# Kernel optimization log

Measured on AMD Instinct MI355X. Metric: run time of the kernel, lower is better.

Reference implementation:

```python
import jax, jax.numpy as jnp
import numpy as np

B, T, D = 8, 2048, 1024
EPS = 1e-5

def _layernorm(x, g, b):
    mu = jnp.mean(x, axis=-1, keepdims=True)
    var = jnp.mean(jnp.square(x - mu), axis=-1, keepdims=True)
    return (x - mu) * jax.lax.rsqrt(var + EPS) * g + b

def setup_inputs() -> dict:
    key = jax.random.key(0)
    ks = jax.random.split(key, 8)
    scale = 1.0 / np.sqrt(D)
    text_inputs = jax.random.normal(ks[0], (B, T, D), dtype=jnp.float32)
    sit_mask = jax.random.randint(ks[1], (B, T), 0, 2).astype(jnp.float32)
    Wq = jax.random.normal(ks[2], (D, D), dtype=jnp.float32) * scale
    Wk = jax.random.normal(ks[3], (D, D), dtype=jnp.float32) * scale
    Wv = jax.random.normal(ks[4], (D, D), dtype=jnp.float32) * scale
    Wf1 = jax.random.normal(ks[5], (D, D), dtype=jnp.float32) * scale
    bf1 = jnp.zeros((D,), dtype=jnp.float32)
    Wf2 = jax.random.normal(ks[6], (D, D), dtype=jnp.float32) * scale
    bf2 = jnp.zeros((D,), dtype=jnp.float32)
    ln1_g = jnp.ones((D,), dtype=jnp.float32)
    ln1_b = jnp.zeros((D,), dtype=jnp.float32)
    ln2_g = jnp.ones((D,), dtype=jnp.float32)
    ln2_b = jnp.zeros((D,), dtype=jnp.float32)
    return dict(text_inputs=text_inputs, sit_mask=sit_mask, Wq=Wq, Wk=Wk, Wv=Wv,
                ln1_g=ln1_g, ln1_b=ln1_b, Wf1=Wf1, bf1=bf1, Wf2=Wf2, bf2=bf2,
                ln2_g=ln2_g, ln2_b=ln2_b)

def reference(text_inputs, sit_mask, Wq, Wk, Wv, ln1_g, ln1_b, Wf1, bf1, Wf2, bf2, ln2_g, ln2_b):
    x = text_inputs  # [B,T,D]
    d = x.shape[-1]
    # torch Linear: y = x @ W.T
    q = jnp.einsum('btd,ed->bte', x, Wq)
    k = jnp.einsum('btd,ed->bte', x, Wk)
    v = jnp.einsum('btd,ed->bte', x, Wv)
    # scaled scores with causal (strictly-upper = -inf) mask
    scores = jnp.einsum('btd,bsd->bts', q, k) / jnp.sqrt(jnp.asarray(d, x.dtype))
    causal = jnp.tril(jnp.ones((x.shape[1], x.shape[1]), dtype=bool))  # keep diag + past
    scores = jnp.where(causal[None], scores, -jnp.inf)
    attn = jax.nn.softmax(scores, axis=-1)
    # per-batch SIT padding mask applied AFTER softmax (rows may not sum to 1)
    pad_keep = (sit_mask[:, :, None] * sit_mask[:, None, :]) != 0  # [B,T,T]
    attn = jnp.where(pad_keep, attn, 0.0)
    att_out = jnp.einsum('bts,bsd->btd', attn, v)
    # residual + LN, FFN (Linear-ReLU-Linear), residual + LN
    h = _layernorm(att_out + x, ln1_g, ln1_b)
    ff = jnp.einsum('btd,ed->bte', jax.nn.relu(jnp.einsum('btd,ed->bte', h, Wf1) + bf1), Wf2) + bf2
    out = _layernorm(ff + h, ln2_g, ln2_b)
    return out
```

## Files before the change

### kernel.cpp

```cpp
#include <hip/hip_runtime.h>

typedef unsigned short ushort_t;
typedef __attribute__((ext_vector_type(8))) __bf16 bf16x8;
typedef __attribute__((ext_vector_type(4))) float f32x4;
typedef __attribute__((ext_vector_type(4))) int i32x4;
typedef __attribute__((ext_vector_type(4))) unsigned short u16x4;

__device__ __forceinline__ float bf2f(ushort_t u) {
  union { unsigned u32; float f; } c; c.u32 = ((unsigned)u) << 16; return c.f;
}
__device__ __forceinline__ ushort_t f2bf(float f) {
  union { float f; unsigned u32; } c; c.f = f;
  unsigned u = c.u32;
  u += 0x7fffu + ((u >> 16) & 1u);
  return (ushort_t)(u >> 16);
}

__device__ __forceinline__ void gload_lds16(const void* g, void* l) {
  __builtin_amdgcn_global_load_lds(
      (const __attribute__((address_space(1))) void*)g,
      (__attribute__((address_space(3))) void*)l,
      16, 0, 0);
}

__device__ __forceinline__ void stage_half(const char* gbase, long row0, int ldbytes,
                                           int kbyte, char* lds_half, int tid)
{
  const int rl = tid >> 3;
  const int cs = ((tid & 7) ^ (rl & 7)) << 4;
  const char* g0 = gbase + (row0 + rl) * (long)ldbytes + kbyte + cs;
  char* l0 = lds_half + ((tid >> 6) << 10);
  gload_lds16(g0, l0);
  gload_lds16(g0 + (long)ldbytes * 64, l0 + 8192);
}

#define FENCE() asm volatile("" ::: "memory")
#define BARX() do { FENCE(); __builtin_amdgcn_sched_barrier(0); \
  __builtin_amdgcn_s_barrier(); __builtin_amdgcn_sched_barrier(0); FENCE(); } while (0)
#define VMW4() do { FENCE(); asm volatile("s_waitcnt vmcnt(4)" ::: "memory"); FENCE(); } while (0)
#define PR1() __builtin_amdgcn_s_setprio(1)
#define PR0() __builtin_amdgcn_s_setprio(0)

#define READ_A(dst, Abase, mb) \
  _Pragma("unroll") for (int m_ = 0; m_ < 4; ++m_) { \
    const char* p_ = (Abase) + ((wr << 7) + (mb) + m_ * 16 + fr) * 128; \
    dst[m_][0] = *(const bf16x8*)(p_ + ch0); \
    dst[m_][1] = *(const bf16x8*)(p_ + ch1); }

#define READ_B(dst, Bbase, jb) \
  _Pragma("unroll") for (int n_ = 0; n_ < 2; ++n_) { \
    const char* p_ = (Bbase) + ((wc << 6) + (jb) + n_ * 16 + fr) * 128; \
    dst[n_][0] = *(const bf16x8*)(p_ + ch0); \
    dst[n_][1] = *(const bf16x8*)(p_ + ch1); }

#define MFMA_Q(ib, jb, aarr, barr) \
  _Pragma("unroll") for (int m_ = 0; m_ < 4; ++m_) \
  _Pragma("unroll") for (int n_ = 0; n_ < 2; ++n_) \
  _Pragma("unroll") for (int s_ = 0; s_ < 2; ++s_) \
    acc[(ib) + m_][(jb) + n_] = __builtin_amdgcn_mfma_f32_16x16x32_bf16( \
        aarr[m_][s_], barr[n_][s_], acc[(ib) + m_][(jb) + n_], 0, 0, 0);

#define STAGE_A(t, h, db) stage_half(gA, m0 + (h) * 128, ldab, (t) << 7, \
    (char*)lds + (db) * 32768 + (h) * 16384, tid)
#define STAGE_B(t, h, db) stage_half(gB, n0 + (h) * 128, ldbb, (t) << 7, \
    (char*)lds + 65536 + (db) * 32768 + (h) * 16384, tid)

template<int EPI, bool TRI, bool CKLIM>
__global__ __launch_bounds__(512, 2) void gemm256(
    const ushort_t* __restrict__ A, int lda, long bsA,
    const ushort_t* __restrict__ B, int ldb, long bsB,
    ushort_t* __restrict__ C, int ldc, long bsC,
    const float* __restrict__ bias, float scale, int K)
{
  __shared__ __attribute__((aligned(16))) ushort_t lds[65536];

  int bx, by;
  if (TRI) {
    int bid = blockIdx.x; by = 0;
    while ((by + 1) * (by + 2) / 2 <= bid) ++by;
    bx = bid - by * (by + 1) / 2;
  } else { bx = blockIdx.x; by = blockIdx.y; }
  const int bz = blockIdx.z;
  const int NT = CKLIM ? ((by + 1) << 2) : (K >> 6);
  const int NIT = NT >> 1, NTm1 = NT - 1;

  const int tid = threadIdx.x;
  const int lane = tid & 63, fr = lane & 15, g = lane >> 4, lm = lane & 7;
  const int wv = tid >> 6, wr = wv >> 2, wc = wv & 3;
  const long m0 = (long)by << 8, n0 = (long)bx << 8;

  const char* gA = (const char*)(A + bz * bsA);
  const char* gB = (const char*)(B + bz * bsB);
  const int ldab = lda << 1, ldbb = ldb << 1;

  const int ch0 = (g ^ lm) << 4;
  const int ch1 = ((4 | g) ^ lm) << 4;

  const char* A0 = (const char*)lds;
  const char* A1 = (const char*)lds + 32768;
  const char* B0 = (const char*)lds + 65536;
  const char* B1 = (const char*)lds + 98304;

  f32x4 acc[8][4] = {};
  bf16x8 aF[4][2], aG[4][2], bX[2][2];

  STAGE_A(0, 0, 0); STAGE_A(0, 1, 0); STAGE_B(0, 0, 0); STAGE_B(0, 1, 0);
  STAGE_A(1, 0, 1); STAGE_A(1, 1, 1);
  VMW4(); BARX();

  for (int i = 0; i < NIT; ++i) {
    const int t1 = 2 * i + 1;
    const int t2 = (2 * i + 2 < NTm1) ? 2 * i + 2 : NTm1;
    const int t3 = (2 * i + 3 < NTm1) ? 2 * i + 3 : NTm1;

    READ_A(aF, A0, 0); READ_B(bX, B0, 0);
    STAGE_B(t1, 0, 1);
    BARX(); PR1(); MFMA_Q(0, 0, aF, bX); PR0(); BARX();
    READ_A(aG, A0, 64);
    STAGE_B(t1, 1, 1);
    BARX(); PR1(); MFMA_Q(4, 0, aG, bX); PR0(); BARX();
    READ_B(bX, B0, 32);
    STAGE_A(t2, 0, 0);
    BARX(); PR1(); MFMA_Q(4, 2, aG, bX); PR0(); BARX();
    STAGE_A(t2, 1, 0);
    BARX(); PR1(); MFMA_Q(0, 2, aF, bX); PR0(); VMW4(); BARX();
    READ_A(aF, A1, 0); READ_B(bX, B1, 0);
    STAGE_B(t2, 0, 0);
    BARX(); PR1(); MFMA_Q(0, 0, aF, bX); PR0(); BARX();
    READ_A(aG, A1, 64);
    STAGE_B(t2, 1, 0);
    BARX(); PR1(); MFMA_Q(4, 0, aG, bX); PR0(); BARX();
    READ_B(bX, B1, 32);
    STAGE_A(t3, 0, 1);
    BARX(); PR1(); MFMA_Q(4, 2, aG, bX); PR0(); BARX();
    STAGE_A(t3, 1, 1);
    BARX(); PR1(); MFMA_Q(0, 2, aF, bX); PR0(); VMW4(); BARX();
  }

  ushort_t* Cb = C + bz * bsC;
  const int cm = g << 2, cn = fr;
#pragma unroll
  for (int i2 = 0; i2 < 8; ++i2)
#pragma unroll
    for (int j2 = 0; j2 < 4; ++j2) {
      const long gm = m0 + (wr << 7) + i2 * 16 + cm;
      const long gn = n0 + (wc << 6) + j2 * 16 + cn;
      float bv = 0.f;
      if constexpr (EPI >= 1) bv = bias[gn];
#pragma unroll
      for (int r = 0; r < 4; ++r) {
        float v = acc[i2][j2][r] * scale + bv;
        if constexpr (EPI == 2) v = fmaxf(v, 0.f);
        Cb[(gm + r) * ldc + gn] = f2bf(v);
      }
    }
}

__global__ __launch_bounds__(256) void transpose_bf16(
    const ushort_t* __restrict__ V, int ldv, long bsV,
    ushort_t* __restrict__ Vt, int ldt, long bsT)
{
  __shared__ __attribute__((aligned(16))) ushort_t tile[64][72];
  const int bz = blockIdx.z;
  const ushort_t* Vb = V + bz * bsV;
  ushort_t* Tb = Vt + bz * bsT;
  const long s0 = (long)blockIdx.y << 6;
  const long d0 = (long)blockIdx.x << 6;
  const int tid = threadIdx.x;
  const int r = tid >> 3, c = tid & 7;
#pragma unroll
  for (int h = 0; h < 2; ++h) {
    const int rr = r + h * 32;
    i32x4 v = *(const i32x4*)(Vb + (s0 + rr) * ldv + d0 + c * 8);
    *(i32x4*)&tile[rr][c * 8] = v;
  }
  __syncthreads();
#pragma unroll
  for (int h = 0; h < 2; ++h) {
    const int dr = r + h * 32;
    union { ushort_t u[8]; i32x4 v; } t;
#pragma unroll
    for (int j = 0; j < 8; ++j) t.u[j] = tile[c * 8 + j][dr];
    *(i32x4*)(Tb + (d0 + dr) * ldt + s0 + c * 8) = t.v;
  }
}

__global__ __launch_bounds__(256) void softmax_sit(ushort_t* __restrict__ S,
                                                   const float* __restrict__ sit)
{
  __shared__ float buf[2048];
  __shared__ float red[4];
  const long row = blockIdx.x;
  const int b = (int)(row >> 11);
  const int t = (int)(row & 2047);
  ushort_t* Srow = S + (row << 11);
  const int tid = threadIdx.x;
  const int n = t + 1;

  float mloc = -3.0e38f;
  for (int i = tid; i < n; i += 256) {
    float v = bf2f(Srow[i]);
    buf[i] = v;
    mloc = fmaxf(mloc, v);
  }
#pragma unroll
  for (int o = 32; o > 0; o >>= 1) mloc = fmaxf(mloc, __shfl_down(mloc, o, 64));
  if ((tid & 63) == 0) red[tid >> 6] = mloc;
  __syncthreads();
  const float m = fmaxf(fmaxf(red[0], red[1]), fmaxf(red[2], red[3]));
  __syncthreads();

  float sloc = 0.f;
  for (int i = tid; i < n; i += 256) sloc += __expf(buf[i] - m);
#pragma unroll
  for (int o = 32; o > 0; o >>= 1) sloc += __shfl_down(sloc, o, 64);
  if ((tid & 63) == 0) red[tid >> 6] = sloc;
  __syncthreads();
  const float l = red[0] + red[1] + red[2] + red[3];

  float inv = 1.f / l;
  if (sit[row] == 0.f) inv = 0.f;
  const float* sitb = sit + ((long)b << 11);
  const int rup = ((t >> 8) + 1) << 8;
  for (int i = tid; i < rup; i += 256) {
    float p = 0.f;
    if (i < n && sitb[i] != 0.f) p = __expf(buf[i] - m) * inv;
    Srow[i] = f2bf(p);
  }
}

template<bool RES_F32, bool OUT_F32>
__global__ __launch_bounds__(256) void resid_ln(
    const ushort_t* __restrict__ xin, const void* __restrict__ resv,
    const float* __restrict__ g, const float* __restrict__ be, void* __restrict__ outv)
{
  __shared__ float red[4];
  const long base = (long)blockIdx.x << 10;
  const int tid = threadIdx.x;
  const int i0 = tid << 2;

  const u16x4 xa = *(const u16x4*)(xin + base + i0);
  float v[4];
  if constexpr (RES_F32) {
    const float4 rv = *(const float4*)((const float*)resv + base + i0);
    v[0] = bf2f(xa.x) + rv.x; v[1] = bf2f(xa.y) + rv.y;
    v[2] = bf2f(xa.z) + rv.z; v[3] = bf2f(xa.w) + rv.w;
  } else {
    const u16x4 rb = *(const u16x4*)((const ushort_t*)resv + base + i0);
    v[0] = bf2f(xa.x) + bf2f(rb.x); v[1] = bf2f(xa.y) + bf2f(rb.y);
    v[2] = bf2f(xa.z) + bf2f(rb.z); v[3] = bf2f(xa.w) + bf2f(rb.w);
  }
  float s = v[0] + v[1] + v[2] + v[3];
#pragma unroll
  for (int o = 32; o > 0; o >>= 1) s += __shfl_down(s, o, 64);
  if ((tid & 63) == 0) red[tid >> 6] = s;
  __syncthreads();
  const float mu = (red[0] + red[1] + red[2] + red[3]) * (1.f / 1024.f);
  __syncthreads();
  float s2 = 0.f;
#pragma unroll
  for (int j = 0; j < 4; ++j) { const float d = v[j] - mu; s2 += d * d; }
#pragma unroll
  for (int o = 32; o > 0; o >>= 1) s2 += __shfl_down(s2, o, 64);
  if ((tid & 63) == 0) red[tid >> 6] = s2;
  __syncthreads();
  const float rstd = rsqrtf((red[0] + red[1] + red[2] + red[3]) * (1.f / 1024.f) + 1e-5f);

  const float4 gv = *(const float4*)(g + i0);
  const float4 bv = *(const float4*)(be + i0);
  const float o0 = (v[0] - mu) * rstd * gv.x + bv.x;
  const float o1 = (v[1] - mu) * rstd * gv.y + bv.y;
  const float o2 = (v[2] - mu) * rstd * gv.z + bv.z;
  const float o3 = (v[3] - mu) * rstd * gv.w + bv.w;
  if constexpr (OUT_F32) {
    float4 ov; ov.x = o0; ov.y = o1; ov.z = o2; ov.w = o3;
    *(float4*)((float*)outv + base + i0) = ov;
  } else {
    u16x4 ob = { f2bf(o0), f2bf(o1), f2bf(o2), f2bf(o3) };
    *(u16x4*)((ushort_t*)outv + base + i0) = ob;
  }
}

__global__ __launch_bounds__(256) void cast_f32_bf16(const float* __restrict__ src,
                                                     ushort_t* __restrict__ dst, int n4)
{
  const int i = blockIdx.x * 256 + threadIdx.x;
  if (i >= n4) return;
  const float4 v = *(const float4*)(src + ((long)i << 2));
  u16x4 o = { f2bf(v.x), f2bf(v.y), f2bf(v.z), f2bf(v.w) };
  *(u16x4*)(dst + ((long)i << 2)) = o;
}

extern "C" void kernel_launch(void* const* d_in, const int* in_sizes, int n_in,
                              void* d_out, int out_size, void* d_ws, size_t ws_size,
                              hipStream_t stream) {
  const int T = 2048, D = 1024;
  const long TD = (long)T * D;
  const long ND = 8 * TD;
  const float* x    = (const float*)d_in[0];
  const float* sit  = (const float*)d_in[1];
  const float* Wq   = (const float*)d_in[2];
  const float* Wk   = (const float*)d_in[3];
  const float* Wv   = (const float*)d_in[4];
  const float* ln1g = (const float*)d_in[5];
  const float* ln1b = (const float*)d_in[6];
  const float* Wf1  = (const float*)d_in[7];
  const float* bf1  = (const float*)d_in[8];
  const float* Wf2  = (const float*)d_in[9];
  const float* bf2  = (const float*)d_in[10];
  const float* ln2g = (const float*)d_in[11];
  const float* ln2b = (const float*)d_in[12];

  ushort_t* W16 = (ushort_t*)d_ws;
  ushort_t* xb  = W16;
  ushort_t* vb  = W16 + ND;
  ushort_t* S   = W16;
  ushort_t* hb  = W16;
  ushort_t* ff1 = W16 + ND;
  ushort_t* vt  = W16 + 2 * ND;
  ushort_t* ff2 = vt;
  ushort_t* wq  = W16 + 3 * ND;
  ushort_t* wk  = wq + (long)D * D;
  ushort_t* wv  = wk + (long)D * D;
  ushort_t* wf1 = wv + (long)D * D;
  ushort_t* wf2 = wf1 + (long)D * D;
  ushort_t* qb = (ushort_t*)d_out;
  ushort_t* kb = qb + ND;
  ushort_t* attb = (ushort_t*)d_out;

  cast_f32_bf16<<<16384, 256, 0, stream>>>(x, xb, (int)(ND / 4));
  cast_f32_bf16<<<1024, 256, 0, stream>>>(Wq, wq, D * D / 4);
  cast_f32_bf16<<<1024, 256, 0, stream>>>(Wk, wk, D * D / 4);
  cast_f32_bf16<<<1024, 256, 0, stream>>>(Wv, wv, D * D / 4);
  cast_f32_bf16<<<1024, 256, 0, stream>>>(Wf1, wf1, D * D / 4);
  cast_f32_bf16<<<1024, 256, 0, stream>>>(Wf2, wf2, D * D / 4);

  gemm256<0, false, false><<<dim3(4, 64, 1), 512, 0, stream>>>(
      xb, 1024, 0, wq, 1024, 0, qb, 1024, 0, nullptr, 1.f, 1024);
  gemm256<0, false, false><<<dim3(4, 64, 1), 512, 0, stream>>>(
      xb, 1024, 0, wk, 1024, 0, kb, 1024, 0, nullptr, 1.f, 1024);
  gemm256<0, false, false><<<dim3(4, 64, 1), 512, 0, stream>>>(
      xb, 1024, 0, wv, 1024, 0, vb, 1024, 0, nullptr, 1.f, 1024);

  transpose_bf16<<<dim3(16, 32, 8), 256, 0, stream>>>(
      vb, 1024, TD, vt, 2048, TD);

  gemm256<0, true, false><<<dim3(36, 1, 8), 512, 0, stream>>>(
      qb, 1024, TD, kb, 1024, TD, S, 2048, (long)T * T, nullptr, 0.03125f, 1024);

  softmax_sit<<<16384, 256, 0, stream>>>(S, sit);

  gemm256<0, false, true><<<dim3(4, 8, 8), 512, 0, stream>>>(
      S, 2048, (long)T * T, vt, 2048, TD, attb, 1024, TD, nullptr, 1.f, 2048);

  resid_ln<true, false><<<16384, 256, 0, stream>>>(attb, x, ln1g, ln1b, hb);

  gemm256<2, false, false><<<dim3(4, 64, 1), 512, 0, stream>>>(
      hb, 1024, 0, wf1, 1024, 0, ff1, 1024, 0, bf1, 1.f, 1024);
  gemm256<1, false, false><<<dim3(4, 64, 1), 512, 0, stream>>>(
      ff1, 1024, 0, wf2, 1024, 0, ff2, 1024, 0, bf2, 1.f, 1024);

  resid_ln<false, true><<<16384, 256, 0, stream>>>(ff2, hb, ln2g, ln2b, (float*)d_out);
}
```

Baseline: 429.1 us.

## Add 256x128 batched GEMM, swizzled block order, vectorized softmax, fused weight casts

```diff
diff --git a/kernel.cpp b/kernel.cpp
--- a/kernel.cpp
+++ b/kernel.cpp
@@ -5,6 +5,7 @@
 typedef __attribute__((ext_vector_type(4))) float f32x4;
 typedef __attribute__((ext_vector_type(4))) int i32x4;
 typedef __attribute__((ext_vector_type(4))) unsigned short u16x4;
+typedef __attribute__((ext_vector_type(8))) unsigned short u16x8;
 
 __device__ __forceinline__ float bf2f(ushort_t u) {
   union { unsigned u32; float f; } c; c.u32 = ((unsigned)u) << 16; return c.f;
@@ -34,10 +35,10 @@
   gload_lds16(g0 + (long)ldbytes * 64, l0 + 8192);
 }
 
-#define FENCE() asm volatile("" ::: "memory")
-#define BARX() do { FENCE(); __builtin_amdgcn_sched_barrier(0); \
-  __builtin_amdgcn_s_barrier(); __builtin_amdgcn_sched_barrier(0); FENCE(); } while (0)
-#define VMW4() do { FENCE(); asm volatile("s_waitcnt vmcnt(4)" ::: "memory"); FENCE(); } while (0)
+#define BAR() __builtin_amdgcn_s_barrier()
+#define VMW4() asm volatile("s_waitcnt vmcnt(4)" ::: "memory")
+#define VMW2() asm volatile("s_waitcnt vmcnt(2)" ::: "memory")
+#define VMW6() asm volatile("s_waitcnt vmcnt(6)" ::: "memory")
 #define PR1() __builtin_amdgcn_s_setprio(1)
 #define PR0() __builtin_amdgcn_s_setprio(0)
 
@@ -47,7 +48,7 @@
     dst[m_][0] = *(const bf16x8*)(p_ + ch0); \
     dst[m_][1] = *(const bf16x8*)(p_ + ch1); }
 
-#define READ_B(dst, Bbase, jb) \
+#define READ_B4(dst, Bbase, jb) \
   _Pragma("unroll") for (int n_ = 0; n_ < 2; ++n_) { \
     const char* p_ = (Bbase) + ((wc << 6) + (jb) + n_ * 16 + fr) * 128; \
     dst[n_][0] = *(const bf16x8*)(p_ + ch0); \
@@ -65,29 +66,148 @@
 #define STAGE_B(t, h, db) stage_half(gB, n0 + (h) * 128, ldbb, (t) << 7, \
     (char*)lds + 65536 + (db) * 32768 + (h) * 16384, tid)
 
-template<int EPI, bool TRI, bool CKLIM>
-__global__ __launch_bounds__(512, 2) void gemm256(
+template<int EPI, bool SWZ>
+__global__ __launch_bounds__(512, 1) void gemm256(
+    const ushort_t* __restrict__ A, int lda,
+    const ushort_t* __restrict__ B, int ldb,
+    ushort_t* __restrict__ C, int ldc,
+    const float* __restrict__ bias, float scale, int K)
+{
+  __shared__ __attribute__((aligned(16))) ushort_t lds[65536];
+
+  int bx, by;
+  if (SWZ) {
+    const int flat = blockIdx.y * 4 + blockIdx.x;
+    by = ((flat >> 5) << 3) | (flat & 7);
+    bx = (flat >> 3) & 3;
+  } else { bx = blockIdx.x; by = blockIdx.y; }
+
+  const int NT = K >> 6;
+  const int NIT = NT >> 1, NTm1 = NT - 1;
+
+  const int tid = threadIdx.x;
+  const int lane = tid & 63, fr = lane & 15, g = lane >> 4, lm = lane & 7;
+  const int wv = tid >> 6, wr = wv >> 2, wc = wv & 3;
+  const long m0 = (long)by << 8, n0 = (long)bx << 8;
+
+  const char* gA = (const char*)A;
+  const char* gB = (const char*)B;
+  const int ldab = lda << 1, ldbb = ldb << 1;
+
+  const int ch0 = (g ^ lm) << 4;
+  const int ch1 = ((4 | g) ^ lm) << 4;
+
+  const char* A0 = (const char*)lds;
+  const char* A1 = (const char*)lds + 32768;
+  const char* B0 = (const char*)lds + 65536;
+  const char* B1 = (const char*)lds + 98304;
+
+  f32x4 acc[8][4] = {};
+  bf16x8 aF[4][2], aG[4][2], bX[2][2];
+
+  STAGE_A(0, 0, 0); STAGE_A(0, 1, 0); STAGE_B(0, 0, 0); STAGE_B(0, 1, 0);
+  STAGE_A(1, 0, 1); STAGE_A(1, 1, 1);
+  VMW4(); BAR();
+
+  for (int i = 0; i < NIT; ++i) {
+    const int t1 = 2 * i + 1;
+    const int t2 = (2 * i + 2 < NTm1) ? 2 * i + 2 : NTm1;
+    const int t3 = (2 * i + 3 < NTm1) ? 2 * i + 3 : NTm1;
+
+    READ_A(aF, A0, 0); READ_B4(bX, B0, 0);
+    STAGE_B(t1, 0, 1);
+    BAR(); PR1(); MFMA_Q(0, 0, aF, bX); PR0(); BAR();
+
+    READ_A(aG, A0, 64);
+    STAGE_B(t1, 1, 1);
+    BAR(); PR1(); MFMA_Q(4, 0, aG, bX); PR0(); BAR();
+
+    READ_B4(bX, B0, 32);
+    STAGE_A(t2, 0, 0);
+    BAR(); PR1(); MFMA_Q(4, 2, aG, bX); PR0(); BAR();
+
+    STAGE_A(t2, 1, 0);
+    BAR(); PR1(); MFMA_Q(0, 2, aF, bX); PR0(); VMW4(); BAR();
+
+    READ_A(aF, A1, 0); READ_B4(bX, B1, 0);
+    STAGE_B(t2, 0, 0);
+    BAR(); PR1(); MFMA_Q(0, 0, aF, bX); PR0(); BAR();
+
+    READ_A(aG, A1, 64);
+    STAGE_B(t2, 1, 0);
+    BAR(); PR1(); MFMA_Q(4, 0, aG, bX); PR0(); BAR();
+
+    READ_B4(bX, B1, 32);
+    STAGE_A(t3, 0, 1);
+    BAR(); PR1(); MFMA_Q(4, 2, aG, bX); PR0(); BAR();
+
+    STAGE_A(t3, 1, 1);
+    BAR(); PR1(); MFMA_Q(0, 2, aF, bX); PR0(); VMW4(); BAR();
+  }
+
+  const int cm = g << 2, cn = fr;
+#pragma unroll
+  for (int i2 = 0; i2 < 8; ++i2)
+#pragma unroll
+    for (int j2 = 0; j2 < 4; ++j2) {
+      const long gm = m0 + (wr << 7) + i2 * 16 + cm;
+      const long gn = n0 + (wc << 6) + j2 * 16 + cn;
+      float bv = 0.f;
+      if constexpr (EPI >= 1) bv = bias[gn];
+#pragma unroll
+      for (int r = 0; r < 4; ++r) {
+        float v = acc[i2][j2][r] * scale + bv;
+        if constexpr (EPI == 2) v = fmaxf(v, 0.f);
+        C[(gm + r) * ldc + gn] = f2bf(v);
+      }
+    }
+}
+
+#define READ_B2(dst, Bbase) \
+  _Pragma("unroll") for (int n_ = 0; n_ < 2; ++n_) { \
+    const char* p_ = (Bbase) + ((wc << 5) + n_ * 16 + fr) * 128; \
+    dst[n_][0] = *(const bf16x8*)(p_ + ch0); \
+    dst[n_][1] = *(const bf16x8*)(p_ + ch1); }
+
+#define MFMA_H(ib, aarr) \
+  _Pragma("unroll") for (int m_ = 0; m_ < 4; ++m_) \
+  _Pragma("unroll") for (int n_ = 0; n_ < 2; ++n_) \
+  _Pragma("unroll") for (int s_ = 0; s_ < 2; ++s_) \
+    acc[(ib) + m_][n_] = __builtin_amdgcn_mfma_f32_16x16x32_bf16( \
+        aarr[m_][s_], bX[n_][s_], acc[(ib) + m_][n_], 0, 0, 0);
+
+#define SA_(t, h, db) stage_half(gA, m0 + (h) * 128, ldab, (t) << 7, \
+    (char*)lds + (db) * 32768 + (h) * 16384, tid)
+#define SB_(t, db) stage_half(gB, n0, ldbb, (t) << 7, \
+    (char*)lds + 65536 + (db) * 16384, tid)
+
+template<int EPI, int MAP, bool CKLIM>
+__global__ __launch_bounds__(512, 1) void gemmA(
     const ushort_t* __restrict__ A, int lda, long bsA,
     const ushort_t* __restrict__ B, int ldb, long bsB,
     ushort_t* __restrict__ C, int ldc, long bsC,
     const float* __restrict__ bias, float scale, int K)
 {
-  __shared__ __attribute__((aligned(16))) ushort_t lds[65536];
-
-  int bx, by;
-  if (TRI) {
-    int bid = blockIdx.x; by = 0;
-    while ((by + 1) * (by + 2) / 2 <= bid) ++by;
-    bx = bid - by * (by + 1) / 2;
-  } else { bx = blockIdx.x; by = blockIdx.y; }
-  const int bz = blockIdx.z;
+  __shared__ __attribute__((aligned(16))) ushort_t lds[49152];
+
+  int bx, by, bz;
+  if (MAP == 1) {
+    const int bid = blockIdx.x;
+    bz = bid / 72; int r = bid % 72;
+    by = 0; while ((by + 1) * (by + 2) <= r) ++by;
+    bx = r - by * (by + 1);
+  } else if (MAP == 2) {
+    const int bid = blockIdx.x;
+    by = 7 - (bid >> 6); bx = (bid >> 3) & 7; bz = bid & 7;
+  } else { bx = blockIdx.x; by = blockIdx.y; bz = blockIdx.z; }
+
   const int NT = CKLIM ? ((by + 1) << 2) : (K >> 6);
   const int NIT = NT >> 1, NTm1 = NT - 1;
 
   const int tid = threadIdx.x;
   const int lane = tid & 63, fr = lane & 15, g = lane >> 4, lm = lane & 7;
   const int wv = tid >> 6, wr = wv >> 2, wc = wv & 3;
-  const long m0 = (long)by << 8, n0 = (long)bx << 8;
+  const long m0 = (long)by << 8, n0 = (long)bx << 7;
 
   const char* gA = (const char*)(A + bz * bsA);
   const char* gB = (const char*)(B + bz * bsB);
@@ -96,45 +216,35 @@
   const int ch0 = (g ^ lm) << 4;
   const int ch1 = ((4 | g) ^ lm) << 4;
 
-  const char* A0 = (const char*)lds;
-  const char* A1 = (const char*)lds + 32768;
-  const char* B0 = (const char*)lds + 65536;
-  const char* B1 = (const char*)lds + 98304;
-
-  f32x4 acc[8][4] = {};
+  const char* A0b = (const char*)lds;
+  const char* A1b = (const char*)lds + 32768;
+  const char* B0b = (const char*)lds + 65536;
+  const char* B1b = (const char*)lds + 81920;
+
+  f32x4 acc[8][2] = {};
   bf16x8 aF[4][2], aG[4][2], bX[2][2];
 
-  STAGE_A(0, 0, 0); STAGE_A(0, 1, 0); STAGE_B(0, 0, 0); STAGE_B(0, 1, 0);
-  STAGE_A(1, 0, 1); STAGE_A(1, 1, 1);
-  VMW4(); BARX();
+  SA_(0, 0, 0); SA_(0, 1, 0); SB_(0, 0); SB_(1, 1);
+  VMW2(); BAR();
 
   for (int i = 0; i < NIT; ++i) {
-    const int t1 = 2 * i + 1;
+    const int o = 2 * i + 1;
     const int t2 = (2 * i + 2 < NTm1) ? 2 * i + 2 : NTm1;
     const int t3 = (2 * i + 3 < NTm1) ? 2 * i + 3 : NTm1;
 
-    READ_A(aF, A0, 0); READ_B(bX, B0, 0);
-    STAGE_B(t1, 0, 1);
-    BARX(); PR1(); MFMA_Q(0, 0, aF, bX); PR0(); BARX();
-    READ_A(aG, A0, 64);
-    STAGE_B(t1, 1, 1);
-    BARX(); PR1(); MFMA_Q(4, 0, aG, bX); PR0(); BARX();
-    READ_B(bX, B0, 32);
-    STAGE_A(t2, 0, 0);
-    BARX(); PR1(); MFMA_Q(4, 2, aG, bX); PR0(); BARX();
-    STAGE_A(t2, 1, 0);
-    BARX(); PR1(); MFMA_Q(0, 2, aF, bX); PR0(); VMW4(); BARX();
-    READ_A(aF, A1, 0); READ_B(bX, B1, 0);
-    STAGE_B(t2, 0, 0);
-    BARX(); PR1(); MFMA_Q(0, 0, aF, bX); PR0(); BARX();
-    READ_A(aG, A1, 64);
-    STAGE_B(t2, 1, 0);
-    BARX(); PR1(); MFMA_Q(4, 0, aG, bX); PR0(); BARX();
-    READ_B(bX, B1, 32);
-    STAGE_A(t3, 0, 1);
-    BARX(); PR1(); MFMA_Q(4, 2, aG, bX); PR0(); BARX();
-    STAGE_A(t3, 1, 1);
-    BARX(); PR1(); MFMA_Q(0, 2, aF, bX); PR0(); VMW4(); BARX();
+    READ_A(aF, A0b, 0); READ_B2(bX, B0b);
+    SA_(o, 0, 1); SA_(o, 1, 1);
+    BAR(); PR1(); MFMA_H(0, aF); PR0(); BAR();
+    READ_A(aG, A0b, 64);
+    SB_(t2, 0);
+    BAR(); PR1(); MFMA_H(4, aG); PR0(); VMW2(); BAR();
+    READ_A(aF, A1b, 0); READ_B2(bX, B1b);
+    SA_(t2, 0, 0);
+    BAR(); PR1(); MFMA_H(0, aF); PR0(); BAR();
+    READ_A(aG, A1b, 64);
+    SA_(t2, 1, 0);
+    SB_(t3, 1);
+    BAR(); PR1(); MFMA_H(4, aG); PR0(); VMW2(); BAR();
   }
 
   ushort_t* Cb = C + bz * bsC;
@@ -142,9 +252,9 @@
 #pragma unroll
   for (int i2 = 0; i2 < 8; ++i2)
 #pragma unroll
-    for (int j2 = 0; j2 < 4; ++j2) {
+    for (int j2 = 0; j2 < 2; ++j2) {
       const long gm = m0 + (wr << 7) + i2 * 16 + cm;
-      const long gn = n0 + (wc << 6) + j2 * 16 + cn;
+      const long gn = n0 + (wc << 5) + j2 * 16 + cn;
       float bv = 0.f;
       if constexpr (EPI >= 1) bv = bias[gn];
 #pragma unroll
@@ -188,21 +298,23 @@
 __global__ __launch_bounds__(256) void softmax_sit(ushort_t* __restrict__ S,
                                                    const float* __restrict__ sit)
 {
-  __shared__ float buf[2048];
   __shared__ float red[4];
   const long row = blockIdx.x;
   const int b = (int)(row >> 11);
   const int t = (int)(row & 2047);
+  const int n = t + 1;
   ushort_t* Srow = S + (row << 11);
   const int tid = threadIdx.x;
-  const int n = t + 1;
+  const int i0 = tid << 3;
+
+  const u16x8 raw = *(const u16x8*)(Srow + i0);
+  float v[8];
+#pragma unroll
+  for (int j = 0; j < 8; ++j) v[j] = bf2f(raw[j]);
 
   float mloc = -3.0e38f;
-  for (int i = tid; i < n; i += 256) {
-    float v = bf2f(Srow[i]);
-    buf[i] = v;
-    mloc = fmaxf(mloc, v);
-  }
+#pragma unroll
+  for (int j = 0; j < 8; ++j) if (i0 + j < n) mloc = fmaxf(mloc, v[j]);
 #pragma unroll
   for (int o = 32; o > 0; o >>= 1) mloc = fmaxf(mloc, __shfl_down(mloc, o, 64));
   if ((tid & 63) == 0) red[tid >> 6] = mloc;
@@ -210,8 +322,13 @@
   const float m = fmaxf(fmaxf(red[0], red[1]), fmaxf(red[2], red[3]));
   __syncthreads();
 
+  float e[8];
   float sloc = 0.f;
-  for (int i = tid; i < n; i += 256) sloc += __expf(buf[i] - m);
+#pragma unroll
+  for (int j = 0; j < 8; ++j) {
+    e[j] = (i0 + j < n) ? __expf(v[j] - m) : 0.f;
+    sloc += e[j];
+  }
 #pragma unroll
   for (int o = 32; o > 0; o >>= 1) sloc += __shfl_down(sloc, o, 64);
   if ((tid & 63) == 0) red[tid >> 6] = sloc;
@@ -220,12 +337,16 @@
 
   float inv = 1.f / l;
   if (sit[row] == 0.f) inv = 0.f;
-  const float* sitb = sit + ((long)b << 11);
   const int rup = ((t >> 8) + 1) << 8;
-  for (int i = tid; i < rup; i += 256) {
-    float p = 0.f;
-    if (i < n && sitb[i] != 0.f) p = __expf(buf[i] - m) * inv;
-    Srow[i] = f2bf(p);
+  if (i0 < rup) {
+    const float* sitb = sit + ((long)b << 11) + i0;
+    u16x8 out;
+#pragma unroll
+    for (int j = 0; j < 8; ++j) {
+      const float p = (i0 + j < n && sitb[j] != 0.f) ? e[j] * inv : 0.f;
+      out[j] = f2bf(p);
+    }
+    *(u16x8*)(Srow + i0) = out;
   }
 }
 
@@ -289,6 +410,20 @@
   const float4 v = *(const float4*)(src + ((long)i << 2));
   u16x4 o = { f2bf(v.x), f2bf(v.y), f2bf(v.z), f2bf(v.w) };
   *(u16x4*)(dst + ((long)i << 2)) = o;
+}
+
+__global__ __launch_bounds__(256) void cast_w5(
+    const float* __restrict__ s0, const float* __restrict__ s1,
+    const float* __restrict__ s2, const float* __restrict__ s3,
+    const float* __restrict__ s4, ushort_t* __restrict__ dst)
+{
+  const int w = blockIdx.y;
+  const float* src = (w == 0) ? s0 : (w == 1) ? s1 : (w == 2) ? s2 : (w == 3) ? s3 : s4;
+  const long off = (long)w << 20;
+  const int i = blockIdx.x * 256 + threadIdx.x;
+  const float4 v = *(const float4*)(src + ((long)i << 2));
+  u16x4 o = { f2bf(v.x), f2bf(v.y), f2bf(v.z), f2bf(v.w) };
+  *(u16x4*)(dst + off + ((long)i << 2)) = o;
 }
 
 extern "C" void kernel_launch(void* const* d_in, const int* in_sizes, int n_in,
@@ -329,36 +464,26 @@
   ushort_t* attb = (ushort_t*)d_out;
 
   cast_f32_bf16<<<16384, 256, 0, stream>>>(x, xb, (int)(ND / 4));
-  cast_f32_bf16<<<1024, 256, 0, stream>>>(Wq, wq, D * D / 4);
-  cast_f32_bf16<<<1024, 256, 0, stream>>>(Wk, wk, D * D / 4);
-  cast_f32_bf16<<<1024, 256, 0, stream>>>(Wv, wv, D * D / 4);
-  cast_f32_bf16<<<1024, 256, 0, stream>>>(Wf1, wf1, D * D / 4);
-  cast_f32_bf16<<<1024, 256, 0, stream>>>(Wf2, wf2, D * D / 4);
-
-  gemm256<0, false, false><<<dim3(4, 64, 1), 512, 0, stream>>>(
-      xb, 1024, 0, wq, 1024, 0, qb, 1024, 0, nullptr, 1.f, 1024);
-  gemm256<0, false, false><<<dim3(4, 64, 1), 512, 0, stream>>>(
-      xb, 1024, 0, wk, 1024, 0, kb, 1024, 0, nullptr, 1.f, 1024);
-  gemm256<0, false, false><<<dim3(4, 64, 1), 512, 0, stream>>>(
-      xb, 1024, 0, wv, 1024, 0, vb, 1024, 0, nullptr, 1.f, 1024);
-
-  transpose_bf16<<<dim3(16, 32, 8), 256, 0, stream>>>(
-      vb, 1024, TD, vt, 2048, TD);
-
-  gemm256<0, true, false><<<dim3(36, 1, 8), 512, 0, stream>>>(
+  cast_w5<<<dim3(1024, 5), 256, 0, stream>>>(Wq, Wk, Wv, Wf1, Wf2, wq);
+
+  gemm256<0, true><<<dim3(4, 64), 512, 0, stream>>>(xb, 1024, wq, 1024, qb, 1024, nullptr, 1.f, 1024);
+  gemm256<0, true><<<dim3(4, 64), 512, 0, stream>>>(xb, 1024, wk, 1024, kb, 1024, nullptr, 1.f, 1024);
+  gemm256<0, true><<<dim3(4, 64), 512, 0, stream>>>(xb, 1024, wv, 1024, vb, 1024, nullptr, 1.f, 1024);
+
+  transpose_bf16<<<dim3(16, 32, 8), 256, 0, stream>>>(vb, 1024, TD, vt, 2048, TD);
+
+  gemmA<0, 1, false><<<dim3(576), 512, 0, stream>>>(
       qb, 1024, TD, kb, 1024, TD, S, 2048, (long)T * T, nullptr, 0.03125f, 1024);
 
   softmax_sit<<<16384, 256, 0, stream>>>(S, sit);
 
-  gemm256<0, false, true><<<dim3(4, 8, 8), 512, 0, stream>>>(
+  gemmA<0, 2, true><<<dim3(512), 512, 0, stream>>>(
       S, 2048, (long)T * T, vt, 2048, TD, attb, 1024, TD, nullptr, 1.f, 2048);
 
   resid_ln<true, false><<<16384, 256, 0, stream>>>(attb, x, ln1g, ln1b, hb);
 
-  gemm256<2, false, false><<<dim3(4, 64, 1), 512, 0, stream>>>(
-      hb, 1024, 0, wf1, 1024, 0, ff1, 1024, 0, bf1, 1.f, 1024);
-  gemm256<1, false, false><<<dim3(4, 64, 1), 512, 0, stream>>>(
-      ff1, 1024, 0, wf2, 1024, 0, ff2, 1024, 0, bf2, 1.f, 1024);
+  gemm256<2, true><<<dim3(4, 64), 512, 0, stream>>>(hb, 1024, wf1, 1024, ff1, 1024, bf1, 1.f, 1024);
+  gemm256<1, true><<<dim3(4, 64), 512, 0, stream>>>(ff1, 1024, wf2, 1024, ff2, 1024, bf2, 1.f, 1024);
 
   resid_ln<false, true><<<16384, 256, 0, stream>>>(ff2, hb, ln2g, ln2b, (float*)d_out);
 }
```

Measured after the change: 401.5 us. -6.4%, faster.
